# Kernel optimization log

Measured on AMD Instinct MI355X. Metric: run time of the kernel, lower is better.

The kernel has to match this reference:

```python
import jax, jax.numpy as jnp
import numpy as np

N_NODES = 100000
N_EDGES = 1600000
N_GRAPHS = 256
D_IN = 128
D_HID = 128
D_OUT = 10
N_GIN_LAYERS = 4  # num_layers - 1
BN_EPS = 1e-5


def setup_inputs() -> dict:
    key = jax.random.key(0)
    ks = jax.random.split(key, 16)
    x = jax.random.normal(ks[0], (N_NODES, D_IN), dtype=jnp.float32)
    edge_src = jax.random.randint(ks[1], (N_EDGES,), 0, N_NODES)
    edge_dst = jax.random.randint(ks[2], (N_EDGES,), 0, N_NODES)
    graph_ids = jnp.sort(jax.random.randint(ks[3], (N_NODES,), 0, N_GRAPHS))
    s = 1.0 / np.sqrt(D_HID)
    # stacked per-layer params (all layers 128->128 since input_dim == hidden_dim)
    W1 = jax.random.normal(ks[4], (N_GIN_LAYERS, D_HID, D_HID), dtype=jnp.float32) * s
    b1 = jnp.zeros((N_GIN_LAYERS, D_HID), dtype=jnp.float32)
    g1 = jnp.ones((N_GIN_LAYERS, D_HID), dtype=jnp.float32)
    bt1 = jnp.zeros((N_GIN_LAYERS, D_HID), dtype=jnp.float32)
    W2 = jax.random.normal(ks[5], (N_GIN_LAYERS, D_HID, D_HID), dtype=jnp.float32) * s
    b2 = jnp.zeros((N_GIN_LAYERS, D_HID), dtype=jnp.float32)
    g2 = jnp.ones((N_GIN_LAYERS, D_HID), dtype=jnp.float32)
    bt2 = jnp.zeros((N_GIN_LAYERS, D_HID), dtype=jnp.float32)
    eps = jnp.zeros((N_GIN_LAYERS,), dtype=jnp.float32)          # learn_eps params
    fusion_w = jnp.ones((N_GIN_LAYERS,), dtype=jnp.float32)      # self.weight
    Wp = jax.random.normal(ks[6], (D_HID, D_OUT), dtype=jnp.float32) * s
    bp = jnp.zeros((D_OUT,), dtype=jnp.float32)
    return {"x": x, "edge_src": edge_src, "edge_dst": edge_dst, "graph_ids": graph_ids,
            "eps": eps, "fusion_w": fusion_w, "W1": W1, "b1": b1, "g1": g1, "bt1": bt1,
            "W2": W2, "b2": b2, "g2": g2, "bt2": bt2, "Wp": Wp, "bp": bp}


def _batchnorm(h, gamma, beta):
    # training-mode BatchNorm1d over node axis
    m = jnp.mean(h, axis=0)
    v = jnp.var(h, axis=0)
    return (h - m) * jax.lax.rsqrt(v + BN_EPS) * gamma + beta


def reference(x, edge_src, edge_dst, graph_ids, eps, fusion_w,
              W1, b1, g1, bt1, W2, b2, g2, bt2, Wp, bp):
    h = x
    hiddens = []
    for l in range(N_GIN_LAYERS):
        # sum neighbor aggregation (spmm with learn_eps -> no self loops in Adj)
        pooled = jax.ops.segment_sum(h[edge_src], edge_dst, num_segments=N_NODES)
        pooled = pooled + (1.0 + eps[l]) * h
        # 2-layer MLP: Linear -> BN -> ReLU -> Linear
        t = jax.nn.relu(_batchnorm(pooled @ W1[l] + b1[l], g1[l], bt1[l]))
        t = t @ W2[l] + b2[l]
        # outer BatchNorm + ReLU
        h = jax.nn.relu(_batchnorm(t, g2[l], bt2[l]))
        hiddens.append(h)
    # attention_global, attention_type == 'weight': weighted sum of 4 hidden scales
    fused = (fusion_w[0] * hiddens[0] + fusion_w[1] * hiddens[1]
             + fusion_w[2] * hiddens[2] + fusion_w[3] * hiddens[3])
    # graph sum pooling (graph_pool spmm) then final linear (dropout = eval identity)
    pooled_g = jax.ops.segment_sum(fused, graph_ids, num_segments=N_GRAPHS)
    return pooled_g @ Wp + bp
```

## Files before the change

kernel.cpp:

```cpp
#include <hip/hip_runtime.h>

#define D 128
#define DOUT 10
#define CT_STRIDE 152
#define TSTR 136

typedef float f32x4 __attribute__((ext_vector_type(4)));
typedef __bf16 bf16x8 __attribute__((ext_vector_type(8)));
typedef unsigned short u16;

__device__ __forceinline__ float bf2f(u16 u) {
    return __uint_as_float(((unsigned int)u) << 16);
}
__device__ __forceinline__ u16 f2bf(float f) {
    unsigned int u = __float_as_uint(f);
    u += 0x7fffu + ((u >> 16) & 1u);
    return (u16)(u >> 16);
}

__global__ void k_zero(float4* __restrict__ p, int n4) {
    int i = blockIdx.x * 256 + threadIdx.x;
    if (i < n4) p[i] = make_float4(0.f, 0.f, 0.f, 0.f);
}

__global__ __launch_bounds__(256) void k_prepw(const float* __restrict__ W1,
                                               const float* __restrict__ W2,
                                               bf16x8* __restrict__ wswz, int L) {
    int b = blockIdx.x >> 3;
    const float* W = (b < L) ? (W1 + (size_t)b * D * D)
                             : (W2 + (size_t)(b - L) * D * D);
    bf16x8* o = wswz + (size_t)b * 2048;
    int idx = ((blockIdx.x & 7) << 8) + threadIdx.x;
    int lane_s = idx & 63;
    int f = idx >> 6;
    int n = ((f >> 2) << 4) | (lane_s & 15);
    int kb = ((f & 3) << 5) | ((lane_s >> 4) << 3);
    bf16x8 fr;
#pragma unroll
    for (int j = 0; j < 8; ++j) fr[j] = (__bf16)W[(kb + j) * D + n];
    o[idx] = fr;
}

__global__ __launch_bounds__(256) void k_hist(const int* __restrict__ dst,
                                              int* __restrict__ cnts, int E, int nb) {
    __shared__ int hist[1024];
    int tid = threadIdx.x;
    for (int i = tid; i < nb; i += 256) hist[i] = 0;
    __syncthreads();
    int e0 = blockIdx.x << 11;
    int e1 = e0 + 2048; if (e1 > E) e1 = E;
    for (int e = e0 + tid; e < e1; e += 256) atomicAdd(&hist[dst[e] >> 7], 1);
    __syncthreads();
    for (int i = tid; i < nb; i += 256) cnts[(blockIdx.x << 10) + i] = hist[i];
}

__global__ __launch_bounds__(256) void k_off(int* __restrict__ cnts,
                                             int* __restrict__ btot,
                                             int nbk, int nb) {
    int wave = threadIdx.x >> 6, lane = threadIdx.x & 63;
    int b = blockIdx.x * 4 + wave;
    if (b >= nb) return;
    int carry = 0;
    for (int base = 0; base < nbk; base += 64) {
        int idx = base + lane;
        int orig = (idx < nbk) ? cnts[(idx << 10) + b] : 0;
        int c = orig;
#pragma unroll
        for (int off = 1; off < 64; off <<= 1) {
            int v = __shfl_up(c, off);
            if (lane >= off) c += v;
        }
        if (idx < nbk) cnts[(idx << 10) + b] = carry + (c - orig);
        carry += __shfl(c, 63);
    }
    if (lane == 0) btot[b] = carry;
}

__global__ __launch_bounds__(256) void k_scat(const int* __restrict__ src,
                                              const int* __restrict__ dst,
                                              const int* __restrict__ cnts,
                                              int* __restrict__ pairs, int E, int nb) {
    __shared__ int lbase[1024];
    __shared__ int lcur[1024];
    int tid = threadIdx.x;
    for (int i = tid; i < nb; i += 256) {
        lbase[i] = cnts[(blockIdx.x << 10) + i];
        lcur[i] = 0;
    }
    __syncthreads();
    int e0 = blockIdx.x << 11;
    int e1 = e0 + 2048; if (e1 > E) e1 = E;
    for (int e = e0 + tid; e < e1; e += 256) {
        int d = dst[e];
        int b = d >> 7;
        int pos = lbase[b] + atomicAdd(&lcur[b], 1);
        if (pos < 4096) pairs[(b << 12) + pos] = (src[e] << 7) | (d & 127);
    }
}

__global__ __launch_bounds__(256) void k_csr(const int* __restrict__ bcnt,
                                             int* __restrict__ pairs,
                                             int* __restrict__ gmeta) {
    __shared__ int lcnt[128], loff[128], lcur[128];
    __shared__ int ledge[4096];
    int b = blockIdx.x, tid = threadIdx.x;
    if (tid < 128) lcnt[tid] = 0;
    __syncthreads();
    int cnt = bcnt[b]; if (cnt > 4096) cnt = 4096;
    const int* pb = pairs + ((size_t)b << 12);
    for (int e = tid; e < cnt; e += 256) atomicAdd(&lcnt[pb[e] & 127], 1);
    __syncthreads();
    if (tid < 128) loff[tid] = lcnt[tid];
    __syncthreads();
    for (int off = 1; off < 128; off <<= 1) {
        int v = 0;
        if (tid < 128 && tid >= off) v = loff[tid - off];
        __syncthreads();
        if (tid < 128) loff[tid] += v;
        __syncthreads();
    }
    if (tid < 128) lcur[tid] = loff[tid] - lcnt[tid];
    __syncthreads();
    for (int e = tid; e < cnt; e += 256) {
        int p = pb[e];
        int pos = atomicAdd(&lcur[p & 127], 1);
        ledge[pos] = p >> 7;
    }
    __syncthreads();
    for (int e = tid; e < cnt; e += 256) pairs[((size_t)b << 12) + e] = ledge[e];
    if (tid < 128) {
        gmeta[(b << 8) + tid] = lcnt[tid];
        gmeta[(b << 8) + 128 + tid] = loff[tid];
    }
}

__global__ void k_gseg(const int* __restrict__ gids, int* __restrict__ gptr,
                       int M, int G) {
    int g = blockIdx.x * blockDim.x + threadIdx.x;
    if (g > G) return;
    if (g == 0) { gptr[0] = 0; return; }
    int lo = 0, hi = M;
    while (lo < hi) {
        int mid = (lo + hi) >> 1;
        if (gids[mid] < g) lo = mid + 1; else hi = mid;
    }
    gptr[g] = lo;
}

__global__ void k_cvt(const float* __restrict__ x, u16* __restrict__ o,
                      int M, int Mpad) {
    long e = ((long)blockIdx.x * 256 + threadIdx.x) * 4;
    if (e >= (long)Mpad * D) return;
    ushort4 r;
    if (e < (long)M * D) {
        float4 v = *(const float4*)(x + e);
        r.x = f2bf(v.x); r.y = f2bf(v.y); r.z = f2bf(v.z); r.w = f2bf(v.w);
    } else {
        r = make_ushort4(0, 0, 0, 0);
    }
    *(ushort4*)(o + e) = r;
}

__global__ __launch_bounds__(512, 6) void k_aggemm(
        const u16* __restrict__ h, const int* __restrict__ gedge,
        const int* __restrict__ gmeta, const int* __restrict__ bcnt,
        const float* __restrict__ eps, int layer,
        const bf16x8* __restrict__ wz, const float* __restrict__ bias,
        u16* __restrict__ O, float* __restrict__ stats, int M) {
    __shared__ union UA {
        struct { int lcnt[128]; int loff[128]; int ledge[4096]; } csr;
        u16 tile[128 * TSTR];
    } shA;
    __shared__ float blds[D], psum[8 * D], psq[8 * D];
    int tid = threadIdx.x;
    int b = blockIdx.x;

    if (tid < 128) shA.csr.lcnt[tid] = gmeta[(b << 8) + tid];
    else if (tid < 256) shA.csr.loff[tid - 128] = gmeta[(b << 8) + tid];
    else if (tid < 256 + D) blds[tid - 256] = bias[tid - 256];
    int cnt = bcnt[b]; if (cnt > 4096) cnt = 4096;
    const int4* ge4 = (const int4*)(gedge + ((size_t)b << 12));
    int n4c = (cnt + 3) >> 2;
    for (int i = tid; i < n4c; i += 512) ((int4*)shA.csr.ledge)[i] = ge4[i];
    __syncthreads();

    float e1 = 1.0f + eps[layer];
    int grp = tid >> 5;
    int c = (tid & 31) << 2;
    float r0[8], r1[8], r2[8], r3[8];
    for (int pass = 0; pass < 8; ++pass) {
        int row = (pass << 4) + grp;
        int node = (b << 7) + row;
        float a0 = 0.f, a1 = 0.f, a2 = 0.f, a3 = 0.f;
        if (node < M) {
            ushort4 sv = *(const ushort4*)(h + ((size_t)node << 7) + c);
            a0 = e1 * bf2f(sv.x); a1 = e1 * bf2f(sv.y);
            a2 = e1 * bf2f(sv.z); a3 = e1 * bf2f(sv.w);
            int dd = shA.csr.lcnt[row];
            int s = shA.csr.loff[row] - dd;
            int i = 0;
            for (; i + 8 <= dd; i += 8) {
                int n0 = shA.csr.ledge[s + i],     n1 = shA.csr.ledge[s + i + 1];
                int n2 = shA.csr.ledge[s + i + 2], n3 = shA.csr.ledge[s + i + 3];
                int n4 = shA.csr.ledge[s + i + 4], n5 = shA.csr.ledge[s + i + 5];
                int n6 = shA.csr.ledge[s + i + 6], n7 = shA.csr.ledge[s + i + 7];
                ushort4 u0 = *(const ushort4*)(h + ((size_t)n0 << 7) + c);
                ushort4 u1 = *(const ushort4*)(h + ((size_t)n1 << 7) + c);
                ushort4 u2 = *(const ushort4*)(h + ((size_t)n2 << 7) + c);
                ushort4 u3 = *(const ushort4*)(h + ((size_t)n3 << 7) + c);
                ushort4 u4 = *(const ushort4*)(h + ((size_t)n4 << 7) + c);
                ushort4 u5 = *(const ushort4*)(h + ((size_t)n5 << 7) + c);
                ushort4 u6 = *(const ushort4*)(h + ((size_t)n6 << 7) + c);
                ushort4 u7 = *(const ushort4*)(h + ((size_t)n7 << 7) + c);
                a0 += bf2f(u0.x) + bf2f(u1.x) + bf2f(u2.x) + bf2f(u3.x)
                    + bf2f(u4.x) + bf2f(u5.x) + bf2f(u6.x) + bf2f(u7.x);
                a1 += bf2f(u0.y) + bf2f(u1.y) + bf2f(u2.y) + bf2f(u3.y)
                    + bf2f(u4.y) + bf2f(u5.y) + bf2f(u6.y) + bf2f(u7.y);
                a2 += bf2f(u0.z) + bf2f(u1.z) + bf2f(u2.z) + bf2f(u3.z)
                    + bf2f(u4.z) + bf2f(u5.z) + bf2f(u6.z) + bf2f(u7.z);
                a3 += bf2f(u0.w) + bf2f(u1.w) + bf2f(u2.w) + bf2f(u3.w)
                    + bf2f(u4.w) + bf2f(u5.w) + bf2f(u6.w) + bf2f(u7.w);
            }
            for (; i + 4 <= dd; i += 4) {
                int n0 = shA.csr.ledge[s + i],     n1 = shA.csr.ledge[s + i + 1];
                int n2 = shA.csr.ledge[s + i + 2], n3 = shA.csr.ledge[s + i + 3];
                ushort4 u0 = *(const ushort4*)(h + ((size_t)n0 << 7) + c);
                ushort4 u1 = *(const ushort4*)(h + ((size_t)n1 << 7) + c);
                ushort4 u2 = *(const ushort4*)(h + ((size_t)n2 << 7) + c);
                ushort4 u3 = *(const ushort4*)(h + ((size_t)n3 << 7) + c);
                a0 += bf2f(u0.x) + bf2f(u1.x) + bf2f(u2.x) + bf2f(u3.x);
                a1 += bf2f(u0.y) + bf2f(u1.y) + bf2f(u2.y) + bf2f(u3.y);
                a2 += bf2f(u0.z) + bf2f(u1.z) + bf2f(u2.z) + bf2f(u3.z);
                a3 += bf2f(u0.w) + bf2f(u1.w) + bf2f(u2.w) + bf2f(u3.w);
            }
            for (; i < dd; ++i) {
                int n0 = shA.csr.ledge[s + i];
                ushort4 u0 = *(const ushort4*)(h + ((size_t)n0 << 7) + c);
                a0 += bf2f(u0.x); a1 += bf2f(u0.y); a2 += bf2f(u0.z); a3 += bf2f(u0.w);
            }
        }
        r0[pass] = a0; r1[pass] = a1; r2[pass] = a2; r3[pass] = a3;
    }
    __syncthreads();

#pragma unroll
    for (int pass = 0; pass < 8; ++pass) {
        int row = (pass << 4) + grp;
        ushort4 v;
        v.x = f2bf(r0[pass]); v.y = f2bf(r1[pass]);
        v.z = f2bf(r2[pass]); v.w = f2bf(r3[pass]);
        *(ushort4*)&shA.tile[row * TSTR + c] = v;
    }
    __syncthreads();

    int wave = tid >> 6, lane = tid & 63;
    int m = lane & 15, quad = lane >> 4;
    f32x4 z = {0.f, 0.f, 0.f, 0.f};
    f32x4 acc[8];
#pragma unroll
    for (int t = 0; t < 8; ++t) acc[t] = z;
    const bf16x8* wlp = wz + lane;
#pragma unroll
    for (int kc = 0; kc < 4; ++kc) {
        bf16x8 af = *(const bf16x8*)&shA.tile[(wave * 16 + m) * TSTR + (kc << 5) + (quad << 3)];
        bf16x8 w0 = wlp[(0  | kc) << 6];
        bf16x8 w1 = wlp[(4  | kc) << 6];
        bf16x8 w2 = wlp[(8  | kc) << 6];
        bf16x8 w3 = wlp[(12 | kc) << 6];
        acc[0] = __builtin_amdgcn_mfma_f32_16x16x32_bf16(af, w0, acc[0], 0, 0, 0);
        acc[1] = __builtin_amdgcn_mfma_f32_16x16x32_bf16(af, w1, acc[1], 0, 0, 0);
        acc[2] = __builtin_amdgcn_mfma_f32_16x16x32_bf16(af, w2, acc[2], 0, 0, 0);
        acc[3] = __builtin_amdgcn_mfma_f32_16x16x32_bf16(af, w3, acc[3], 0, 0, 0);
        w0 = wlp[(16 | kc) << 6];
        w1 = wlp[(20 | kc) << 6];
        w2 = wlp[(24 | kc) << 6];
        w3 = wlp[(28 | kc) << 6];
        acc[4] = __builtin_amdgcn_mfma_f32_16x16x32_bf16(af, w0, acc[4], 0, 0, 0);
        acc[5] = __builtin_amdgcn_mfma_f32_16x16x32_bf16(af, w1, acc[5], 0, 0, 0);
        acc[6] = __builtin_amdgcn_mfma_f32_16x16x32_bf16(af, w2, acc[6], 0, 0, 0);
        acc[7] = __builtin_amdgcn_mfma_f32_16x16x32_bf16(af, w3, acc[7], 0, 0, 0);
    }
    __syncthreads();

    int lr0 = wave * 16 + (quad << 2);
    int gr0 = (b << 7) + lr0;
#pragma unroll
    for (int t = 0; t < 8; ++t) {
        int cch = (t << 4) | m;
        float bc = blds[cch];
        float s = 0.f, q = 0.f;
#pragma unroll
        for (int r = 0; r < 4; ++r) {
            float v = acc[t][r] + bc;
            shA.tile[(lr0 + r) * TSTR + cch] = f2bf(v);
            if (gr0 + r < M) { s += v; q += v * v; }
        }
        s += __shfl_xor(s, 16); s += __shfl_xor(s, 32);
        q += __shfl_xor(q, 16); q += __shfl_xor(q, 32);
        if (quad == 0) { psum[wave * D + cch] = s; psq[wave * D + cch] = q; }
    }
    __syncthreads();

    int mrow = M - (b << 7);
#pragma unroll
    for (int i = 0; i < 4; ++i) {
        int idx = (i << 9) + tid;
        int row = idx >> 4, ch8 = (idx & 15) << 3;
        if (row < mrow) {
            float4 v = *(const float4*)&shA.tile[row * TSTR + ch8];
            *(float4*)(O + (((size_t)(b << 7) + row) << 7) + ch8) = v;
        }
    }
    if (tid < D) {
        float s = 0.f, q = 0.f;
#pragma unroll
        for (int w = 0; w < 8; ++w) { s += psum[w * D + tid]; q += psq[w * D + tid]; }
        float* st = stats + ((b & 7) << 8);
        atomicAdd(&st[tid], s);
        atomicAdd(&st[D + tid], q);
    }
}

__global__ __launch_bounds__(256, 4) void k_gemm_bn(
        u16* __restrict__ A, const bf16x8* __restrict__ wz,
        const float* __restrict__ bias, const float* __restrict__ stats_in,
        const float* __restrict__ gamma, const float* __restrict__ beta,
        float* __restrict__ stats_out, float invM, int M, int nbuck) {
    int j = blockIdx.x;
    int x = j & 7, n = j >> 3;
    int half = n & 1, q = n >> 1;
    int b = (q << 3) + x;
    if (b >= nbuck) return;
    int rb = (b << 7) + (half << 6);

    __shared__ union { bf16x8 w[2048]; u16 c[64 * CT_STRIDE]; } sh;
    __shared__ float blds[D], s_sc[D], s_sh[D], psum[4 * D], psq[4 * D];
    int tid = threadIdx.x;
    int wave = tid >> 6, lane = tid & 63;
    int m = lane & 15, quad = lane >> 4;
    int row0 = rb + wave * 16;

    const u16* ap = A + (size_t)(row0 + m) * D + (quad << 3);
    ushort4 p[4][2];
#pragma unroll
    for (int kc = 0; kc < 4; ++kc) {
        p[kc][0] = *(const ushort4*)(ap + (kc << 5));
        p[kc][1] = *(const ushort4*)(ap + (kc << 5) + 4);
    }

    for (int i = tid; i < 2048; i += 256) sh.w[i] = wz[i];
    if (tid < D) {
        float s = 0.f, qq = 0.f;
#pragma unroll
        for (int r = 0; r < 8; ++r) {
            s += stats_in[(r << 8) + tid];
            qq += stats_in[(r << 8) + D + tid];
        }
        float mean = s * invM;
        float var = qq * invM - mean * mean;
        float sc = rsqrtf(var + 1e-5f) * gamma[tid];
        s_sc[tid] = sc;
        s_sh[tid] = beta[tid] - mean * sc;
        blds[tid] = bias[tid];
    }
    __syncthreads();

    f32x4 z = {0.f, 0.f, 0.f, 0.f};
    f32x4 acc[8];
#pragma unroll
    for (int t = 0; t < 8; ++t) acc[t] = z;

#pragma unroll
    for (int kc = 0; kc < 4; ++kc) {
        int kb = (kc << 5) | (quad << 3);
        float4 c0 = *(const float4*)&s_sc[kb];
        float4 c1 = *(const float4*)&s_sc[kb + 4];
        float4 h0 = *(const float4*)&s_sh[kb];
        float4 h1 = *(const float4*)&s_sh[kb + 4];
        ushort4 p0 = p[kc][0], p1 = p[kc][1];
        bf16x8 af;
        af[0] = (__bf16)fmaxf(0.f, fmaf(bf2f(p0.x), c0.x, h0.x));
        af[1] = (__bf16)fmaxf(0.f, fmaf(bf2f(p0.y), c0.y, h0.y));
        af[2] = (__bf16)fmaxf(0.f, fmaf(bf2f(p0.z), c0.z, h0.z));
        af[3] = (__bf16)fmaxf(0.f, fmaf(bf2f(p0.w), c0.w, h0.w));
        af[4] = (__bf16)fmaxf(0.f, fmaf(bf2f(p1.x), c1.x, h1.x));
        af[5] = (__bf16)fmaxf(0.f, fmaf(bf2f(p1.y), c1.y, h1.y));
        af[6] = (__bf16)fmaxf(0.f, fmaf(bf2f(p1.z), c1.z, h1.z));
        af[7] = (__bf16)fmaxf(0.f, fmaf(bf2f(p1.w), c1.w, h1.w));
#pragma unroll
        for (int t = 0; t < 8; ++t)
            acc[t] = __builtin_amdgcn_mfma_f32_16x16x32_bf16(
                af, sh.w[(((t << 2) | kc) << 6) | lane], acc[t], 0, 0, 0);
    }
    __syncthreads();

    int lr0 = wave * 16 + (quad << 2);
    int gr0 = rb + lr0;
#pragma unroll
    for (int t = 0; t < 8; ++t) {
        int cch = (t << 4) | m;
        float bc = blds[cch];
        float s = 0.f, qq = 0.f;
#pragma unroll
        for (int r = 0; r < 4; ++r) {
            float v = acc[t][r] + bc;
            sh.c[(lr0 + r) * CT_STRIDE + cch] = f2bf(v);
            if (gr0 + r < M) { s += v; qq += v * v; }
        }
        s += __shfl_xor(s, 16); s += __shfl_xor(s, 32);
        qq += __shfl_xor(qq, 16); qq += __shfl_xor(qq, 32);
        if (quad == 0) { psum[wave * D + cch] = s; psq[wave * D + cch] = qq; }
    }
    __syncthreads();

    int mrow = M - rb;
#pragma unroll
    for (int i = 0; i < 4; ++i) {
        int idx = (i << 8) + tid;
        int row = idx >> 4, ch8 = (idx & 15) << 3;
        if (row < mrow) {
            float4 v = *(const float4*)&sh.c[row * CT_STRIDE + ch8];
            *(float4*)(A + ((size_t)(rb + row) << 7) + ch8) = v;
        }
    }
    if (tid < D) {
        float s = psum[tid] + psum[D + tid] + psum[2 * D + tid] + psum[3 * D + tid];
        float qq = psq[tid] + psq[D + tid] + psq[2 * D + tid] + psq[3 * D + tid];
        float* st = stats_out + (x << 8);
        atomicAdd(&st[tid], s);
        atomicAdd(&st[D + tid], qq);
    }
}

__device__ __forceinline__ void bnrow(const u16* __restrict__ y,
                                      u16* __restrict__ hout, size_t row, int c,
                                      float4 sc4, float4 sh4, int writeh,
                                      float& a0, float& a1, float& a2, float& a3) {
    ushort4 u = *(const ushort4*)(y + (row << 7) + c);
    float h0 = fmaxf(0.f, fmaf(bf2f(u.x), sc4.x, sh4.x));
    float h1 = fmaxf(0.f, fmaf(bf2f(u.y), sc4.y, sh4.y));
    float h2 = fmaxf(0.f, fmaf(bf2f(u.z), sc4.z, sh4.z));
    float h3 = fmaxf(0.f, fmaf(bf2f(u.w), sc4.w, sh4.w));
    if (writeh) {
        ushort4 o;
        o.x = f2bf(h0); o.y = f2bf(h1); o.z = f2bf(h2); o.w = f2bf(h3);
        *(ushort4*)(hout + (row << 7) + c) = o;
    }
    a0 += h0; a1 += h1; a2 += h2; a3 += h3;
}

template<int WRITEH>
__global__ __launch_bounds__(512) void k_bnpool(
        const u16* __restrict__ y, const float* __restrict__ stats,
        const float* __restrict__ gamma, const float* __restrict__ beta,
        const int* __restrict__ gptr, const float* __restrict__ fw,
        int layer, u16* __restrict__ hout, float* __restrict__ gacc, float invM) {
    __shared__ float s_sc[D], s_sh[D];
    __shared__ float red[16 * D];
    int t = threadIdx.x;
    if (t < D) {
        float s = 0.f, q = 0.f;
#pragma unroll
        for (int r = 0; r < 8; ++r) {
            s += stats[(r << 8) + t];
            q += stats[(r << 8) + D + t];
        }
        float mean = s * invM;
        float sv = rsqrtf(q * invM - mean * mean + 1e-5f) * gamma[t];
        s_sc[t] = sv;
        s_sh[t] = beta[t] - mean * sv;
    }
    __syncthreads();

    int g = blockIdx.x;
    int n0 = gptr[g], n1 = gptr[g + 1];
    int c = (t & 31) << 2;
    int rg = t >> 5;
    float4 sc4 = *(const float4*)&s_sc[c];
    float4 sh4 = *(const float4*)&s_sh[c];

    float a0 = 0.f, a1 = 0.f, a2 = 0.f, a3 = 0.f;
    int r = n0 + rg;
    for (; r + 48 < n1; r += 64) {
        bnrow(y, hout, (size_t)r,        c, sc4, sh4, WRITEH, a0, a1, a2, a3);
        bnrow(y, hout, (size_t)(r + 16), c, sc4, sh4, WRITEH, a0, a1, a2, a3);
        bnrow(y, hout, (size_t)(r + 32), c, sc4, sh4, WRITEH, a0, a1, a2, a3);
        bnrow(y, hout, (size_t)(r + 48), c, sc4, sh4, WRITEH, a0, a1, a2, a3);
    }
    for (; r < n1; r += 16)
        bnrow(y, hout, (size_t)r, c, sc4, sh4, WRITEH, a0, a1, a2, a3);

    *(float4*)&red[rg * D + c] = make_float4(a0, a1, a2, a3);
    __syncthreads();

    if (t < D) {
        float s = 0.f;
#pragma unroll
        for (int w = 0; w < 16; ++w) s += red[w * D + t];
        gacc[((size_t)g << 7) + t] += fw[layer] * s;
    }
}

__global__ void k_final(const float* __restrict__ gacc, const float* __restrict__ Wp,
                        const float* __restrict__ bp, float* __restrict__ out) {
    __shared__ float w[D * DOUT];
    __shared__ float bb[DOUT];
    int t = threadIdx.x;
    for (int i = t; i < D * DOUT; i += blockDim.x) w[i] = Wp[i];
    if (t < DOUT) bb[t] = bp[t];
    __syncthreads();
    float acc[DOUT];
#pragma unroll
    for (int o = 0; o < DOUT; ++o) acc[o] = bb[o];
    for (int k = 0; k < D; ++k) {
        float a = gacc[(size_t)t * D + k];
#pragma unroll
        for (int o = 0; o < DOUT; ++o) acc[o] += a * w[k * DOUT + o];
    }
#pragma unroll
    for (int o = 0; o < DOUT; ++o) out[(size_t)t * DOUT + o] = acc[o];
}

extern "C" void kernel_launch(void* const* d_in, const int* in_sizes, int n_in,
                              void* d_out, int out_size, void* d_ws, size_t ws_size,
                              hipStream_t stream) {
    const float* x    = (const float*)d_in[0];
    const int* esrc   = (const int*)d_in[1];
    const int* edst   = (const int*)d_in[2];
    const int* gids   = (const int*)d_in[3];
    const float* eps  = (const float*)d_in[4];
    const float* fw   = (const float*)d_in[5];
    const float* W1   = (const float*)d_in[6];
    const float* b1   = (const float*)d_in[7];
    const float* g1   = (const float*)d_in[8];
    const float* bt1  = (const float*)d_in[9];
    const float* W2   = (const float*)d_in[10];
    const float* b2   = (const float*)d_in[11];
    const float* g2   = (const float*)d_in[12];
    const float* bt2  = (const float*)d_in[13];
    const float* Wp   = (const float*)d_in[14];
    const float* bp   = (const float*)d_in[15];
    float* out        = (float*)d_out;

    const int M = in_sizes[3];
    const int E = in_sizes[1];
    const int L = in_sizes[4];
    const int G = out_size / DOUT;
    const int nb  = (M + 127) >> 7;
    const int Mpad = nb << 7;
    const int nbk = (E + 2047) >> 11;
    const float invM = 1.0f / (float)M;

    char* ws = (char*)d_ws;
    u16* bufT  = (u16*)ws;  ws += (size_t)Mpad * D * 2;
    u16* bufH  = (u16*)ws;  ws += (size_t)Mpad * D * 2;
    int* pairs = (int*)ws;  ws += (size_t)nb * 4096 * 4;
    int* cnts  = (int*)ws;  ws += (size_t)nbk * 1024 * 4;
    int* btot  = (int*)ws;  ws += 1024 * 4;
    int* gptr  = (int*)ws;  ws += 512 * 4;
    int* gmeta = (int*)ws;  ws += (size_t)nb * 256 * 4;
    bf16x8* wswz = (bf16x8*)ws; ws += (size_t)2 * L * 2048 * 16;
    float* stats = (float*)ws; ws += (size_t)L * 4096 * 4;
    float* gacc  = (float*)ws; ws += (size_t)G * D * 4;

    int zbytes = L * 4096 * 4 + G * D * 4;
    int n4 = zbytes / 16;
    k_zero<<<(n4 + 255) / 256, 256, 0, stream>>>((float4*)stats, n4);

    k_prepw<<<2 * L * 8, 256, 0, stream>>>(W1, W2, wswz, L);
    k_hist<<<nbk, 256, 0, stream>>>(edst, cnts, E, nb);
    k_off<<<(nb + 3) / 4, 256, 0, stream>>>(cnts, btot, nbk, nb);
    k_scat<<<nbk, 256, 0, stream>>>(esrc, edst, cnts, pairs, E, nb);
    k_csr<<<nb, 256, 0, stream>>>(btot, pairs, gmeta);
    k_gseg<<<1, 512, 0, stream>>>(gids, gptr, M, G);
    k_cvt<<<(Mpad * (D / 4) + 255) / 256, 256, 0, stream>>>(x, bufH, M, Mpad);

    int nbR = (nb + 7) & ~7;
    for (int l = 0; l < L; ++l) {
        float* st1 = stats + (size_t)l * 4096;
        float* st2 = st1 + 2048;
        k_aggemm<<<nb, 512, 0, stream>>>(bufH, pairs, gmeta, btot, eps, l,
                                         wswz + (size_t)l * 2048, b1 + (size_t)l * D,
                                         bufT, st1, M);
        k_gemm_bn<<<nbR * 2, 256, 0, stream>>>(bufT, wswz + (size_t)(L + l) * 2048,
                                               b2 + (size_t)l * D, st1,
                                               g1 + (size_t)l * D, bt1 + (size_t)l * D,
                                               st2, invM, M, nb);
        if (l < L - 1)
            k_bnpool<1><<<G, 512, 0, stream>>>(bufT, st2, g2 + (size_t)l * D,
                                               bt2 + (size_t)l * D, gptr, fw, l,
                                               bufH, gacc, invM);
        else
            k_bnpool<0><<<G, 512, 0, stream>>>(bufT, st2, g2 + (size_t)l * D,
                                               bt2 + (size_t)l * D, gptr, fw, l,
                                               bufH, gacc, invM);
    }
    k_final<<<1, G, 0, stream>>>(gacc, Wp, bp, out);
}
```

Measured before the change: 645.4 us.

## Read GEMM weights directly from global and split graph pooling across two blocks

In k_gemm_bn the weight staging into shared memory is removed, and each lane now loads its bf16x8 weight fragments straight from global memory (L2-cached) just before the MFMAs. This drops the LDS fill and shrinks shared memory use, which may allow more blocks per CU, at the cost of repeated global reads of the weights. Separately, k_bnpool now runs two blocks per graph, each taking interleaved row groups and writing its own partial accumulator. k_final sums the two partials, which doubles the parallelism of the pooling pass.

```diff
diff --git a/kernel.cpp b/kernel.cpp
--- a/kernel.cpp
+++ b/kernel.cpp
@@ -333,7 +333,7 @@
     if (b >= nbuck) return;
     int rb = (b << 7) + (half << 6);
 
-    __shared__ union { bf16x8 w[2048]; u16 c[64 * CT_STRIDE]; } sh;
+    __shared__ u16 shc[64 * CT_STRIDE];
     __shared__ float blds[D], s_sc[D], s_sh[D], psum[4 * D], psq[4 * D];
     int tid = threadIdx.x;
     int wave = tid >> 6, lane = tid & 63;
@@ -348,7 +348,6 @@
         p[kc][1] = *(const ushort4*)(ap + (kc << 5) + 4);
     }
 
-    for (int i = tid; i < 2048; i += 256) sh.w[i] = wz[i];
     if (tid < D) {
         float s = 0.f, qq = 0.f;
 #pragma unroll
@@ -369,6 +368,7 @@
     f32x4 acc[8];
 #pragma unroll
     for (int t = 0; t < 8; ++t) acc[t] = z;
+    const bf16x8* wlp = wz + lane;
 
 #pragma unroll
     for (int kc = 0; kc < 4; ++kc) {
@@ -387,10 +387,22 @@
         af[5] = (__bf16)fmaxf(0.f, fmaf(bf2f(p1.y), c1.y, h1.y));
         af[6] = (__bf16)fmaxf(0.f, fmaf(bf2f(p1.z), c1.z, h1.z));
         af[7] = (__bf16)fmaxf(0.f, fmaf(bf2f(p1.w), c1.w, h1.w));
-#pragma unroll
-        for (int t = 0; t < 8; ++t)
-            acc[t] = __builtin_amdgcn_mfma_f32_16x16x32_bf16(
-                af, sh.w[(((t << 2) | kc) << 6) | lane], acc[t], 0, 0, 0);
+        bf16x8 w0 = wlp[(0  | kc) << 6];
+        bf16x8 w1 = wlp[(4  | kc) << 6];
+        bf16x8 w2 = wlp[(8  | kc) << 6];
+        bf16x8 w3 = wlp[(12 | kc) << 6];
+        acc[0] = __builtin_amdgcn_mfma_f32_16x16x32_bf16(af, w0, acc[0], 0, 0, 0);
+        acc[1] = __builtin_amdgcn_mfma_f32_16x16x32_bf16(af, w1, acc[1], 0, 0, 0);
+        acc[2] = __builtin_amdgcn_mfma_f32_16x16x32_bf16(af, w2, acc[2], 0, 0, 0);
+        acc[3] = __builtin_amdgcn_mfma_f32_16x16x32_bf16(af, w3, acc[3], 0, 0, 0);
+        w0 = wlp[(16 | kc) << 6];
+        w1 = wlp[(20 | kc) << 6];
+        w2 = wlp[(24 | kc) << 6];
+        w3 = wlp[(28 | kc) << 6];
+        acc[4] = __builtin_amdgcn_mfma_f32_16x16x32_bf16(af, w0, acc[4], 0, 0, 0);
+        acc[5] = __builtin_amdgcn_mfma_f32_16x16x32_bf16(af, w1, acc[5], 0, 0, 0);
+        acc[6] = __builtin_amdgcn_mfma_f32_16x16x32_bf16(af, w2, acc[6], 0, 0, 0);
+        acc[7] = __builtin_amdgcn_mfma_f32_16x16x32_bf16(af, w3, acc[7], 0, 0, 0);
     }
     __syncthreads();
 
@@ -404,7 +416,7 @@
 #pragma unroll
         for (int r = 0; r < 4; ++r) {
             float v = acc[t][r] + bc;
-            sh.c[(lr0 + r) * CT_STRIDE + cch] = f2bf(v);
+            shc[(lr0 + r) * CT_STRIDE + cch] = f2bf(v);
             if (gr0 + r < M) { s += v; qq += v * v; }
         }
         s += __shfl_xor(s, 16); s += __shfl_xor(s, 32);
@@ -419,7 +431,7 @@
         int idx = (i << 8) + tid;
         int row = idx >> 4, ch8 = (idx & 15) << 3;
         if (row < mrow) {
-            float4 v = *(const float4*)&sh.c[row * CT_STRIDE + ch8];
+            float4 v = *(const float4*)&shc[row * CT_STRIDE + ch8];
             *(float4*)(A + ((size_t)(rb + row) << 7) + ch8) = v;
         }
     }
@@ -472,32 +484,32 @@
     }
     __syncthreads();
 
-    int g = blockIdx.x;
+    int g = blockIdx.x >> 1, half = blockIdx.x & 1;
     int n0 = gptr[g], n1 = gptr[g + 1];
     int c = (t & 31) << 2;
-    int rg = t >> 5;
+    int rg = (half << 4) + (t >> 5);
     float4 sc4 = *(const float4*)&s_sc[c];
     float4 sh4 = *(const float4*)&s_sh[c];
 
     float a0 = 0.f, a1 = 0.f, a2 = 0.f, a3 = 0.f;
     int r = n0 + rg;
-    for (; r + 48 < n1; r += 64) {
+    for (; r + 96 < n1; r += 128) {
         bnrow(y, hout, (size_t)r,        c, sc4, sh4, WRITEH, a0, a1, a2, a3);
-        bnrow(y, hout, (size_t)(r + 16), c, sc4, sh4, WRITEH, a0, a1, a2, a3);
         bnrow(y, hout, (size_t)(r + 32), c, sc4, sh4, WRITEH, a0, a1, a2, a3);
-        bnrow(y, hout, (size_t)(r + 48), c, sc4, sh4, WRITEH, a0, a1, a2, a3);
-    }
-    for (; r < n1; r += 16)
+        bnrow(y, hout, (size_t)(r + 64), c, sc4, sh4, WRITEH, a0, a1, a2, a3);
+        bnrow(y, hout, (size_t)(r + 96), c, sc4, sh4, WRITEH, a0, a1, a2, a3);
+    }
+    for (; r < n1; r += 32)
         bnrow(y, hout, (size_t)r, c, sc4, sh4, WRITEH, a0, a1, a2, a3);
 
-    *(float4*)&red[rg * D + c] = make_float4(a0, a1, a2, a3);
+    *(float4*)&red[(t >> 5) * D + c] = make_float4(a0, a1, a2, a3);
     __syncthreads();
 
     if (t < D) {
         float s = 0.f;
 #pragma unroll
         for (int w = 0; w < 16; ++w) s += red[w * D + t];
-        gacc[((size_t)g << 7) + t] += fw[layer] * s;
+        gacc[((size_t)blockIdx.x << 7) + t] += fw[layer] * s;
     }
 }
 
@@ -513,7 +525,7 @@
 #pragma unroll
     for (int o = 0; o < DOUT; ++o) acc[o] = bb[o];
     for (int k = 0; k < D; ++k) {
-        float a = gacc[(size_t)t * D + k];
+        float a = gacc[((size_t)(t * 2) << 7) + k] + gacc[((size_t)(t * 2 + 1) << 7) + k];
 #pragma unroll
         for (int o = 0; o < DOUT; ++o) acc[o] += a * w[k * DOUT + o];
     }
@@ -561,9 +573,9 @@
     int* gmeta = (int*)ws;  ws += (size_t)nb * 256 * 4;
     bf16x8* wswz = (bf16x8*)ws; ws += (size_t)2 * L * 2048 * 16;
     float* stats = (float*)ws; ws += (size_t)L * 4096 * 4;
-    float* gacc  = (float*)ws; ws += (size_t)G * D * 4;
-
-    int zbytes = L * 4096 * 4 + G * D * 4;
+    float* gacc  = (float*)ws; ws += (size_t)2 * G * D * 4;
+
+    int zbytes = L * 4096 * 4 + 2 * G * D * 4;
     int n4 = zbytes / 16;
     k_zero<<<(n4 + 255) / 256, 256, 0, stream>>>((float4*)stats, n4);
 
@@ -587,13 +599,13 @@
                                                g1 + (size_t)l * D, bt1 + (size_t)l * D,
                                                st2, invM, M, nb);
         if (l < L - 1)
-            k_bnpool<1><<<G, 512, 0, stream>>>(bufT, st2, g2 + (size_t)l * D,
-                                               bt2 + (size_t)l * D, gptr, fw, l,
-                                               bufH, gacc, invM);
+            k_bnpool<1><<<2 * G, 512, 0, stream>>>(bufT, st2, g2 + (size_t)l * D,
+                                                   bt2 + (size_t)l * D, gptr, fw, l,
+                                                   bufH, gacc, invM);
         else
-            k_bnpool<0><<<G, 512, 0, stream>>>(bufT, st2, g2 + (size_t)l * D,
-                                               bt2 + (size_t)l * D, gptr, fw, l,
-                                               bufH, gacc, invM);
+            k_bnpool<0><<<2 * G, 512, 0, stream>>>(bufT, st2, g2 + (size_t)l * D,
+                                                   bt2 + (size_t)l * D, gptr, fw, l,
+                                                   bufH, gacc, invM);
     }
     k_final<<<1, G, 0, stream>>>(gacc, Wp, bp, out);
 }
```

New measurement: 659.6 us. 2.2% more time.
